# Kernel optimization log

Hardware: AMD Instinct MI355X
Metric: run time of the kernel (lower is better)

## Reference

```python
import jax, jax.numpy as jnp
import numpy as np

EPS = 1e-5

def _bn_eval(x, gamma, beta, mean, var):
    return (x - mean) * (gamma / jnp.sqrt(var + EPS)) + beta

def setup_inputs() -> dict:
    key = jax.random.key(0)
    ks = jax.random.split(key, 12)
    N, E, D, C, H = 100000, 1000000, 64, 32, 128
    fused = 4 * D + C  # 288
    z = jax.random.normal(ks[0], (N, D), dtype=jnp.float32)
    edge_index = jax.random.randint(ks[1], (2, E), 0, N, dtype=jnp.int64)
    edge_context = jax.random.normal(ks[2], (E, C), dtype=jnp.float32)
    W1 = jax.random.normal(ks[3], (fused, H), dtype=jnp.float32) / np.sqrt(fused)
    b1 = jnp.zeros((H,), jnp.float32)
    g1 = jnp.ones((H,), jnp.float32); be1 = jnp.zeros((H,), jnp.float32)
    m1 = jnp.zeros((H,), jnp.float32); v1 = jnp.ones((H,), jnp.float32)
    W2 = jax.random.normal(ks[4], (H, H // 2), dtype=jnp.float32) / np.sqrt(H)
    b2 = jnp.zeros((H // 2,), jnp.float32)
    g2 = jnp.ones((H // 2,), jnp.float32); be2 = jnp.zeros((H // 2,), jnp.float32)
    m2 = jnp.zeros((H // 2,), jnp.float32); v2 = jnp.ones((H // 2,), jnp.float32)
    W3 = jax.random.normal(ks[5], (H // 2, 1), dtype=jnp.float32) / np.sqrt(H // 2)
    b3 = jnp.zeros((1,), jnp.float32)
    return {"z": z, "edge_index": edge_index, "edge_context": edge_context,
            "W1": W1, "b1": b1, "g1": g1, "be1": be1, "m1": m1, "v1": v1,
            "W2": W2, "b2": b2, "g2": g2, "be2": be2, "m2": m2, "v2": v2,
            "W3": W3, "b3": b3}

def reference(z, edge_index, edge_context,
              W1, b1, g1, be1, m1, v1,
              W2, b2, g2, be2, m2, v2,
              W3, b3):
    # gather endpoint embeddings: [E, D]
    src = z[edge_index[0]]
    dst = z[edge_index[1]]
    # fused features: [E, 4*D + C]
    fused = jnp.concatenate([src, dst, src * dst, jnp.abs(src - dst), edge_context], axis=1)
    x = jax.nn.relu(_bn_eval(fused @ W1 + b1, g1, be1, m1, v1))
    x = jax.nn.relu(_bn_eval(x @ W2 + b2, g2, be2, m2, v2))
    return (x @ W3 + b3).reshape(-1)
```

## Files before the change

kernel.cpp:

```cpp
#include <hip/hip_runtime.h>
#include <hip/hip_bf16.h>

typedef __attribute__((ext_vector_type(8))) short bf16x8;
typedef __attribute__((ext_vector_type(4))) float f32x4;
typedef __attribute__((ext_vector_type(4))) unsigned int u32x4;
typedef __attribute__((ext_vector_type(2))) unsigned int u32x2;
typedef __attribute__((ext_vector_type(2))) __bf16 bf16x2v;

#define EPS 1e-5f

__device__ inline unsigned short f2bf(float x) {
  unsigned int u = __builtin_bit_cast(unsigned int, x);
  unsigned int r = (u + 0x7FFFu + ((u >> 16) & 1u)) >> 16;
  return (unsigned short)r;
}

__device__ inline unsigned int cvtpk(float a, float b) {
  bf16x2v v = {(__bf16)a, (__bf16)b};
  return __builtin_bit_cast(unsigned int, v);
}

__global__ void prep_kernel(const float* __restrict__ W1, const float* __restrict__ W2,
                            const float* __restrict__ b1, const float* __restrict__ g1,
                            const float* __restrict__ be1, const float* __restrict__ m1,
                            const float* __restrict__ v1,
                            const float* __restrict__ b2, const float* __restrict__ g2,
                            const float* __restrict__ be2, const float* __restrict__ m2,
                            const float* __restrict__ v2,
                            unsigned short* __restrict__ w1f, unsigned short* __restrict__ w2f,
                            float* __restrict__ sc) {
  int t = blockIdx.x * 256 + threadIdx.x;
  if (t < 36864) {
    int j = t & 7, l = (t >> 3) & 63, f = t >> 9;
    int kb = f >> 3, nb = f & 7;
    int rk = kb * 32 + ((l >> 4) << 3) + j;
    int cn = (nb << 4) + (l & 15);
    w1f[t] = f2bf(W1[rk * 128 + cn]);
  } else if (t < 45056) {
    int o = t - 36864;
    int j = o & 7, l = (o >> 3) & 63, f = o >> 9;
    int kb = f >> 2, nb = f & 3;
    int s = kb * 32 + ((l >> 4) << 3) + j;
    int rk = (s & 96) | ((s & 1) << 4) | ((s >> 1) & 15);
    int cn = (nb << 4) + (l & 15);
    w2f[o] = f2bf(W2[rk * 64 + cn]);
  } else if (t < 45184) {
    int j = t - 45056;
    float s = g1[j] * rsqrtf(v1[j] + EPS);
    sc[j] = s;
    sc[128 + j] = (b1[j] - m1[j]) * s + be1[j];
  } else if (t < 45248) {
    int j = t - 45184;
    float s = g2[j] * rsqrtf(v2[j] + EPS);
    sc[256 + j] = s;
    sc[320 + j] = (b2[j] - m2[j]) * s + be2[j];
  }
}

#define R_X1_OFF 81920
#define R_W2_OFF 114688
#define R_L3_OFF 131072
#define R_LDS_TOTAL 132096

#define WRITE_A_R()                                                                              \
  do {                                                                                           \
    const int rswz_ = (sr & 7) << 4;                                                             \
    char* rowp_ = AR + sr * 640;                                                                 \
    u32x4 s0_ = {cvtpk(sv0[0], sv0[1]), cvtpk(sv0[2], sv0[3]), cvtpk(sv1[0], sv1[1]),            \
                 cvtpk(sv1[2], sv1[3])};                                                         \
    u32x4 s1_ = {cvtpk(sv2[0], sv2[1]), cvtpk(sv2[2], sv2[3]), cvtpk(sv3[0], sv3[1]),            \
                 cvtpk(sv3[2], sv3[3])};                                                         \
    u32x4 d0_ = {cvtpk(dv0[0], dv0[1]), cvtpk(dv0[2], dv0[3]), cvtpk(dv1[0], dv1[1]),            \
                 cvtpk(dv1[2], dv1[3])};                                                         \
    u32x4 d1_ = {cvtpk(dv2[0], dv2[1]), cvtpk(dv2[2], dv2[3]), cvtpk(dv3[0], dv3[1]),            \
                 cvtpk(dv3[2], dv3[3])};                                                         \
    u32x4 p0_ = {cvtpk(sv0[0] * dv0[0], sv0[1] * dv0[1]), cvtpk(sv0[2] * dv0[2], sv0[3] * dv0[3]),\
                 cvtpk(sv1[0] * dv1[0], sv1[1] * dv1[1]), cvtpk(sv1[2] * dv1[2], sv1[3] * dv1[3])};\
    u32x4 p1_ = {cvtpk(sv2[0] * dv2[0], sv2[1] * dv2[1]), cvtpk(sv2[2] * dv2[2], sv2[3] * dv2[3]),\
                 cvtpk(sv3[0] * dv3[0], sv3[1] * dv3[1]), cvtpk(sv3[2] * dv3[2], sv3[3] * dv3[3])};\
    u32x4 a0_ = {cvtpk(fabsf(sv0[0] - dv0[0]), fabsf(sv0[1] - dv0[1])),                          \
                 cvtpk(fabsf(sv0[2] - dv0[2]), fabsf(sv0[3] - dv0[3])),                          \
                 cvtpk(fabsf(sv1[0] - dv1[0]), fabsf(sv1[1] - dv1[1])),                          \
                 cvtpk(fabsf(sv1[2] - dv1[2]), fabsf(sv1[3] - dv1[3]))};                         \
    u32x4 a1_ = {cvtpk(fabsf(sv2[0] - dv2[0]), fabsf(sv2[1] - dv2[1])),                          \
                 cvtpk(fabsf(sv2[2] - dv2[2]), fabsf(sv2[3] - dv2[3])),                          \
                 cvtpk(fabsf(sv3[0] - dv3[0]), fabsf(sv3[1] - dv3[1])),                          \
                 cvtpk(fabsf(sv3[2] - dv3[2]), fabsf(sv3[3] - dv3[3]))};                         \
    u32x4 c0_ = {cvtpk(cv0[0], cv0[1]), cvtpk(cv0[2], cv0[3]), cvtpk(cv1[0], cv1[1]),            \
                 cvtpk(cv1[2], cv1[3])};                                                         \
    *(u32x4*)(rowp_ + ((sh * 32) ^ rswz_)) = s0_;                                                \
    *(u32x4*)(rowp_ + ((sh * 32 + 16) ^ rswz_)) = s1_;                                           \
    *(u32x4*)(rowp_ + ((128 + sh * 32) ^ rswz_)) = d0_;                                          \
    *(u32x4*)(rowp_ + ((128 + sh * 32 + 16) ^ rswz_)) = d1_;                                     \
    *(u32x4*)(rowp_ + ((256 + sh * 32) ^ rswz_)) = p0_;                                          \
    *(u32x4*)(rowp_ + ((256 + sh * 32 + 16) ^ rswz_)) = p1_;                                     \
    *(u32x4*)(rowp_ + ((384 + sh * 32) ^ rswz_)) = a0_;                                          \
    *(u32x4*)(rowp_ + ((384 + sh * 32 + 16) ^ rswz_)) = a1_;                                     \
    *(u32x4*)(rowp_ + ((512 + sh * 16) ^ rswz_)) = c0_;                                          \
  } while (0)

#define GATHER_NEXT_R(tg)                                                                        \
  do {                                                                                           \
    const f32x4* zs_ = (const f32x4*)(z + ((size_t)i0n * 64 + sh * 16));                         \
    sv0 = zs_[0]; sv1 = zs_[1]; sv2 = zs_[2]; sv3 = zs_[3];                                      \
    const f32x4* zd_ = (const f32x4*)(z + ((size_t)i1n * 64 + sh * 16));                         \
    dv0 = zd_[0]; dv1 = zd_[1]; dv2 = zd_[2]; dv3 = zd_[3];                                      \
    int eg_ = ((tg) << 7) + sr;                                                                  \
    int esg_ = eg_ < E ? eg_ : E - 1;                                                            \
    const f32x4* cx_ = (const f32x4*)(ctx + (size_t)esg_ * 32 + sh * 8);                         \
    cv0 = cx_[0]; cv1 = cx_[1];                                                                  \
    int tn_ = (tg) + grid;                                                                       \
    if (tn_ >= nblk) tn_ = (tg);                                                                 \
    int en_ = (tn_ << 7) + sr;                                                                   \
    int esn_ = en_ < E ? en_ : E - 1;                                                            \
    i0n = ei[esn_];                                                                              \
    i1n = ei[E + esn_];                                                                          \
  } while (0)

#define MFMA16(A, B, C) __builtin_amdgcn_mfma_f32_16x16x32_bf16((A), (B), (C), 0, 0, 0)

#define L1STEP_R(KB, BB0, BB1)                                                                   \
  do {                                                                                           \
    bf16x8 a0_ = *(const bf16x8*)(ap0 + (((KB) * 64 + g * 16) ^ aswz));                          \
    bf16x8 a1_ = *(const bf16x8*)(ap1 + (((KB) * 64 + g * 16) ^ aswz));                          \
    bf16x8 a2_ = *(const bf16x8*)(ap2 + (((KB) * 64 + g * 16) ^ aswz));                          \
    bf16x8 a3_ = *(const bf16x8*)(ap3 + (((KB) * 64 + g * 16) ^ aswz));                          \
    acc00 = MFMA16(a0_, BB0, acc00); acc01 = MFMA16(a0_, BB1, acc01);                            \
    acc10 = MFMA16(a1_, BB0, acc10); acc11 = MFMA16(a1_, BB1, acc11);                            \
    acc20 = MFMA16(a2_, BB0, acc20); acc21 = MFMA16(a2_, BB1, acc21);                            \
    acc30 = MFMA16(a3_, BB0, acc30); acc31 = MFMA16(a3_, BB1, acc31);                            \
  } while (0)

#define X1W_R(MF, ACA, ACB)                                                                      \
  do {                                                                                           \
    _Pragma("unroll")                                                                            \
    for (int j = 0; j < 4; j++) {                                                                \
      int row_ = wr * 64 + (MF) * 16 + 4 * g + j;                                                \
      unsigned int p_ = cvtpk(fmaxf(ACA[j] * s1v0 + c1v0, 0.f),                                  \
                              fmaxf(ACB[j] * s1v1 + c1v1, 0.f));                                 \
      *(unsigned int*)(X1 + row_ * 256 + (xoff ^ ((row_ & 7) << 4))) = p_;                       \
    }                                                                                            \
  } while (0)

#define L2STEP_R(KB)                                                                             \
  do {                                                                                           \
    bf16x8 xa_ = *(const bf16x8*)(xp0 + (((KB) * 64 + g * 16) ^ aswz));                          \
    bf16x8 xb_ = *(const bf16x8*)(xp1 + (((KB) * 64 + g * 16) ^ aswz));                          \
    bf16x8 bg_ = *(const bf16x8*)(W2L + (((KB) * 4 + w2c * 2 + 0) * 64 + lane) * 16);            \
    bf16x8 bh_ = *(const bf16x8*)(W2L + (((KB) * 4 + w2c * 2 + 1) * 64 + lane) * 16);            \
    acc2A0 = MFMA16(xa_, bg_, acc2A0); acc2A1 = MFMA16(xa_, bh_, acc2A1);                        \
    acc2B0 = MFMA16(xb_, bg_, acc2B0); acc2B1 = MFMA16(xb_, bh_, acc2B1);                        \
  } while (0)

__global__ __launch_bounds__(512, 1) void fused_kernel_r(
    const float* __restrict__ z, const int* __restrict__ ei, const float* __restrict__ ctx,
    const unsigned short* __restrict__ w1f, const unsigned short* __restrict__ w2f,
    const float* __restrict__ sc, const float* __restrict__ w3, const float* __restrict__ b3,
    float* __restrict__ out, int E, int nblk) {
  extern __shared__ char lds[];
  char* AR = lds;
  char* X1 = lds + R_X1_OFF;
  char* W2L = lds + R_W2_OFF;
  float* l3 = (float*)(lds + R_L3_OFF);

  const int tid = threadIdx.x;
  const int lane = tid & 63, wave = tid >> 6;
  const int g = lane >> 4, lq = lane & 15;
  const int wr = wave >> 2, wc = wave & 3;
  const int w2r = wave >> 1, w2c = wave & 1;
  const int sr = tid >> 2, sh = tid & 3;
  const int grid = gridDim.x;
  const int aswz = (lq & 7) << 4;

  ((f32x4*)W2L)[tid] = ((const f32x4*)w2f)[tid];
  ((f32x4*)W2L)[512 + tid] = ((const f32x4*)w2f)[512 + tid];

  const int col0 = wc * 32 + lq;
  const float s1v0 = sc[col0], c1v0 = sc[128 + col0];
  const float s1v1 = sc[col0 + 16], c1v1 = sc[128 + col0 + 16];
  const int colA = w2c * 32 + lq;
  const float s2A = sc[256 + colA], c2A = sc[320 + colA];
  const float s2B = sc[256 + colA + 16], c2B = sc[320 + colA + 16];
  const float w3A = w3[colA], w3B = w3[colA + 16];
  const float b3v = b3[0];
  const int xoff = wc * 64 + lq * 4;

  const bf16x8* W1G = (const bf16x8*)w1f;
  bf16x8 w1r0 = W1G[(0 * 8 + wc * 2 + 0) * 64 + lane], w1s0 = W1G[(0 * 8 + wc * 2 + 1) * 64 + lane];
  bf16x8 w1r1 = W1G[(1 * 8 + wc * 2 + 0) * 64 + lane], w1s1 = W1G[(1 * 8 + wc * 2 + 1) * 64 + lane];
  bf16x8 w1r2 = W1G[(2 * 8 + wc * 2 + 0) * 64 + lane], w1s2 = W1G[(2 * 8 + wc * 2 + 1) * 64 + lane];
  bf16x8 w1r3 = W1G[(3 * 8 + wc * 2 + 0) * 64 + lane], w1s3 = W1G[(3 * 8 + wc * 2 + 1) * 64 + lane];
  bf16x8 w1r4 = W1G[(4 * 8 + wc * 2 + 0) * 64 + lane], w1s4 = W1G[(4 * 8 + wc * 2 + 1) * 64 + lane];
  bf16x8 w1r5 = W1G[(5 * 8 + wc * 2 + 0) * 64 + lane], w1s5 = W1G[(5 * 8 + wc * 2 + 1) * 64 + lane];
  bf16x8 w1r6 = W1G[(6 * 8 + wc * 2 + 0) * 64 + lane], w1s6 = W1G[(6 * 8 + wc * 2 + 1) * 64 + lane];
  bf16x8 w1r7 = W1G[(7 * 8 + wc * 2 + 0) * 64 + lane], w1s7 = W1G[(7 * 8 + wc * 2 + 1) * 64 + lane];
  bf16x8 w1r8 = W1G[(8 * 8 + wc * 2 + 0) * 64 + lane], w1s8 = W1G[(8 * 8 + wc * 2 + 1) * 64 + lane];

  f32x4 sv0, sv1, sv2, sv3, dv0, dv1, dv2, dv3, cv0, cv1;
  int i0n, i1n;
  int t = blockIdx.x;

  {
    int e = (t << 7) + sr;
    int es = e < E ? e : E - 1;
    int a0 = ei[es], a1 = ei[E + es];
    const f32x4* cx = (const f32x4*)(ctx + (size_t)es * 32 + sh * 8);
    cv0 = cx[0]; cv1 = cx[1];
    const f32x4* zs = (const f32x4*)(z + ((size_t)a0 * 64 + sh * 16));
    sv0 = zs[0]; sv1 = zs[1]; sv2 = zs[2]; sv3 = zs[3];
    const f32x4* zd = (const f32x4*)(z + ((size_t)a1 * 64 + sh * 16));
    dv0 = zd[0]; dv1 = zd[1]; dv2 = zd[2]; dv3 = zd[3];
    int tn = t + grid;
    if (tn >= nblk) tn = t;
    int en = (tn << 7) + sr;
    int esn = en < E ? en : E - 1;
    i0n = ei[esn];
    i1n = ei[E + esn];
  }
  WRITE_A_R();
  {
    int tn = t + grid;
    if (tn >= nblk) tn = t;
    GATHER_NEXT_R(tn);
  }
  __syncthreads();

  for (; t < nblk; t += grid) {
    f32x4 acc00 = {0.f, 0.f, 0.f, 0.f}, acc01 = acc00, acc10 = acc00, acc11 = acc00;
    f32x4 acc20 = acc00, acc21 = acc00, acc30 = acc00, acc31 = acc00;
    const char* ap0 = AR + (wr * 64 + 0 * 16 + lq) * 640;
    const char* ap1 = AR + (wr * 64 + 1 * 16 + lq) * 640;
    const char* ap2 = AR + (wr * 64 + 2 * 16 + lq) * 640;
    const char* ap3 = AR + (wr * 64 + 3 * 16 + lq) * 640;
    L1STEP_R(0, w1r0, w1s0);
    L1STEP_R(1, w1r1, w1s1);
    L1STEP_R(2, w1r2, w1s2);
    L1STEP_R(3, w1r3, w1s3);
    L1STEP_R(4, w1r4, w1s4);
    L1STEP_R(5, w1r5, w1s5);
    L1STEP_R(6, w1r6, w1s6);
    L1STEP_R(7, w1r7, w1s7);
    L1STEP_R(8, w1r8, w1s8);
    __syncthreads();

    WRITE_A_R();
    {
      int tn2 = t + 2 * grid;
      if (tn2 >= nblk) tn2 = t + grid < nblk ? t + grid : t;
      GATHER_NEXT_R(tn2);
    }
    X1W_R(0, acc00, acc01);
    X1W_R(1, acc10, acc11);
    X1W_R(2, acc20, acc21);
    X1W_R(3, acc30, acc31);
    __syncthreads();

    f32x4 acc2A0 = {0.f, 0.f, 0.f, 0.f}, acc2A1 = acc2A0, acc2B0 = acc2A0, acc2B1 = acc2A0;
    const char* xp0 = X1 + (w2r * 32 + lq) * 256;
    const char* xp1 = xp0 + 4096;
    L2STEP_R(0);
    L2STEP_R(1);
    L2STEP_R(2);
    L2STEP_R(3);

    {
#pragma unroll
      for (int j = 0; j < 4; j++) {
        float pA = fmaxf(acc2A0[j] * s2A + c2A, 0.f) * w3A +
                   fmaxf(acc2A1[j] * s2B + c2B, 0.f) * w3B;
        pA += __shfl_xor(pA, 1);
        pA += __shfl_xor(pA, 2);
        pA += __shfl_xor(pA, 4);
        pA += __shfl_xor(pA, 8);
        float pB = fmaxf(acc2B0[j] * s2A + c2A, 0.f) * w3A +
                   fmaxf(acc2B1[j] * s2B + c2B, 0.f) * w3B;
        pB += __shfl_xor(pB, 1);
        pB += __shfl_xor(pB, 2);
        pB += __shfl_xor(pB, 4);
        pB += __shfl_xor(pB, 8);
        if (lq == 0) {
          l3[(w2r * 32 + 4 * g + j) * 2 + w2c] = pA;
          l3[(w2r * 32 + 16 + 4 * g + j) * 2 + w2c] = pB;
        }
      }
    }
    __syncthreads();

    if (tid < 128) {
      int e = (t << 7) + tid;
      if (e < E) out[e] = l3[tid * 2] + l3[tid * 2 + 1] + b3v;
    }
  }
}

#define F_SC_OFF 73728
#define F_A_OFF 75776
#define F_L3_OFF 157696
#define F_LDS_TOTAL 158720

#define WRITE_A_F()                                                                              \
  do {                                                                                           \
    const int rswz_ = (sr & 7) << 4;                                                             \
    char* rowp_ = AR + sr * 640;                                                                 \
    u32x4 ps_ = {cvtpk(sv0[0], sv0[1]), cvtpk(sv0[2], sv0[3]), cvtpk(sv1[0], sv1[1]),            \
                 cvtpk(sv1[2], sv1[3])};                                                         \
    u32x4 pd_ = {cvtpk(dv0[0], dv0[1]), cvtpk(dv0[2], dv0[3]), cvtpk(dv1[0], dv1[1]),            \
                 cvtpk(dv1[2], dv1[3])};                                                         \
    u32x4 pp_ = {cvtpk(sv0[0] * dv0[0], sv0[1] * dv0[1]), cvtpk(sv0[2] * dv0[2], sv0[3] * dv0[3]),\
                 cvtpk(sv1[0] * dv1[0], sv1[1] * dv1[1]), cvtpk(sv1[2] * dv1[2], sv1[3] * dv1[3])};\
    u32x4 pa_ = {cvtpk(fabsf(sv0[0] - dv0[0]), fabsf(sv0[1] - dv0[1])),                          \
                 cvtpk(fabsf(sv0[2] - dv0[2]), fabsf(sv0[3] - dv0[3])),                          \
                 cvtpk(fabsf(sv1[0] - dv1[0]), fabsf(sv1[1] - dv1[1])),                          \
                 cvtpk(fabsf(sv1[2] - dv1[2]), fabsf(sv1[3] - dv1[3]))};                         \
    u32x2 pc_ = {cvtpk(cv[0], cv[1]), cvtpk(cv[2], cv[3])};                                      \
    *(u32x4*)(rowp_ + ((sh * 16) ^ rswz_)) = ps_;                                                \
    *(u32x4*)(rowp_ + ((128 + sh * 16) ^ rswz_)) = pd_;                                          \
    *(u32x4*)(rowp_ + ((256 + sh * 16) ^ rswz_)) = pp_;                                          \
    *(u32x4*)(rowp_ + ((384 + sh * 16) ^ rswz_)) = pa_;                                          \
    *(u32x2*)(rowp_ + 512 + ((sh * 8) ^ rswz_)) = pc_;                                           \
  } while (0)

#define GATHER_NEXT_F(tg)                                                                        \
  do {                                                                                           \
    const f32x4* zs_ = (const f32x4*)(z + ((size_t)i0n * 64 + sh * 8));                          \
    sv0 = zs_[0];                                                                                \
    sv1 = zs_[1];                                                                                \
    const f32x4* zd_ = (const f32x4*)(z + ((size_t)i1n * 64 + sh * 8));                          \
    dv0 = zd_[0];                                                                                \
    dv1 = zd_[1];                                                                                \
    int eg_ = ((tg) << 7) + sr;                                                                  \
    int esg_ = eg_ < E ? eg_ : E - 1;                                                            \
    cv = *(const f32x4*)(ctx + (size_t)esg_ * 32 + sh * 4);                                      \
    int tn_ = (tg) + grid;                                                                       \
    if (tn_ >= nblk) tn_ = (tg);                                                                 \
    int en_ = (tn_ << 7) + sr;                                                                   \
    int esn_ = en_ < E ? en_ : E - 1;                                                            \
    i0n = ei[esn_];                                                                              \
    i1n = ei[E + esn_];                                                                          \
  } while (0)

__global__ __launch_bounds__(1024, 4) void fused_kernel_f(
    const float* __restrict__ z, const int* __restrict__ ei, const float* __restrict__ ctx,
    const unsigned short* __restrict__ w1f, const unsigned short* __restrict__ w2f,
    const float* __restrict__ sc, const float* __restrict__ w3, const float* __restrict__ b3,
    float* __restrict__ out, int E, int nblk) {
  extern __shared__ char lds[];
  char* W1L = lds;
  float* SC = (float*)(lds + F_SC_OFF);
  char* AR = lds + F_A_OFF;
  char* X1 = lds + F_A_OFF;
  float* l3 = (float*)(lds + F_L3_OFF);

  const int tid = threadIdx.x;
  const int lane = tid & 63, wave = tid >> 6;
  const int g = lane >> 4, lq = lane & 15;
  const int wr = wave >> 2, wc = wave & 3;
  const int w2r = wave >> 1, w2c = wave & 1;
  const int sr = tid >> 3, sh = tid & 7;
  const int grid = gridDim.x;

  {
    const f32x4* s = (const f32x4*)w1f;
    f32x4* d = (f32x4*)W1L;
#pragma unroll
    for (int i = 0; i < 4; i++) d[i * 1024 + tid] = s[i * 1024 + tid];
    if (tid < 512) d[4096 + tid] = s[4096 + tid];
    if (tid < 128) {
      SC[tid] = sc[tid];
      SC[128 + tid] = sc[128 + tid];
    } else if (tid < 192) {
      int j = tid - 128;
      SC[256 + j] = sc[256 + j];
      SC[320 + j] = sc[320 + j];
      SC[384 + j] = w3[j];
    } else if (tid == 192) {
      SC[448] = b3[0];
    }
  }

  bf16x8 w2g0, w2g1, w2g2, w2g3, w2h0, w2h1, w2h2, w2h3;
  {
    const bf16x8* W2G = (const bf16x8*)w2f;
    w2g0 = W2G[(0 * 4 + w2c * 2 + 0) * 64 + lane];
    w2h0 = W2G[(0 * 4 + w2c * 2 + 1) * 64 + lane];
    w2g1 = W2G[(1 * 4 + w2c * 2 + 0) * 64 + lane];
    w2h1 = W2G[(1 * 4 + w2c * 2 + 1) * 64 + lane];
    w2g2 = W2G[(2 * 4 + w2c * 2 + 0) * 64 + lane];
    w2h2 = W2G[(2 * 4 + w2c * 2 + 1) * 64 + lane];
    w2g3 = W2G[(3 * 4 + w2c * 2 + 0) * 64 + lane];
    w2h3 = W2G[(3 * 4 + w2c * 2 + 1) * 64 + lane];
  }

  f32x4 sv0, sv1, dv0, dv1, cv;
  int i0n, i1n;
  int t = blockIdx.x;

  {
    int e = (t << 7) + sr;
    int es = e < E ? e : E - 1;
    int a0 = ei[es], a1 = ei[E + es];
    cv = *(const f32x4*)(ctx + (size_t)es * 32 + sh * 4);
    const f32x4* zs = (const f32x4*)(z + ((size_t)a0 * 64 + sh * 8));
    sv0 = zs[0];
    sv1 = zs[1];
    const f32x4* zd = (const f32x4*)(z + ((size_t)a1 * 64 + sh * 8));
    dv0 = zd[0];
    dv1 = zd[1];
    int tn = t + grid;
    if (tn >= nblk) tn = t;
    int en = (tn << 7) + sr;
    int esn = en < E ? en : E - 1;
    i0n = ei[esn];
    i1n = ei[E + esn];
  }
  WRITE_A_F();
  {
    int tn = t + grid;
    if (tn >= nblk) tn = t;
    GATHER_NEXT_F(tn);
  }
  __syncthreads();

  for (; t < nblk; t += grid) {
    f32x4 acc00 = {0.f, 0.f, 0.f, 0.f}, acc01 = acc00, acc10 = acc00, acc11 = acc00;
    const bf16x8* W1F = (const bf16x8*)W1L;
    const int row0 = wr * 32 + lq, row1 = row0 + 16;
    const int swz0 = (row0 & 7) << 4, swz1 = (row1 & 7) << 4;
    const char* ap0 = AR + row0 * 640;
    const char* ap1 = AR + row1 * 640;
#pragma unroll
    for (int kb = 0; kb < 9; kb++) {
      bf16x8 a0 = *(const bf16x8*)(ap0 + ((kb * 64 + g * 16) ^ swz0));
      bf16x8 a1 = *(const bf16x8*)(ap1 + ((kb * 64 + g * 16) ^ swz1));
      bf16x8 b0 = W1F[(kb * 8 + wc * 2 + 0) * 64 + lane];
      bf16x8 b1 = W1F[(kb * 8 + wc * 2 + 1) * 64 + lane];
      acc00 = MFMA16(a0, b0, acc00);
      acc01 = MFMA16(a0, b1, acc01);
      acc10 = MFMA16(a1, b0, acc10);
      acc11 = MFMA16(a1, b1, acc11);
    }
    __syncthreads();

    {
      const int col0 = wc * 32 + lq;
      const float s1v0 = SC[col0], c1v0 = SC[128 + col0];
      const float s1v1 = SC[col0 + 16], c1v1 = SC[128 + col0 + 16];
      const int xoff = wc * 64 + lq * 4;
#pragma unroll
      for (int j = 0; j < 4; j++) {
        int rowa = wr * 32 + 4 * g + j;
        unsigned int pA = cvtpk(fmaxf(acc00[j] * s1v0 + c1v0, 0.f),
                                fmaxf(acc01[j] * s1v1 + c1v1, 0.f));
        *(unsigned int*)(X1 + rowa * 256 + (xoff ^ ((rowa & 7) << 4))) = pA;
        int rowb = rowa + 16;
        unsigned int pB = cvtpk(fmaxf(acc10[j] * s1v0 + c1v0, 0.f),
                                fmaxf(acc11[j] * s1v1 + c1v1, 0.f));
        *(unsigned int*)(X1 + rowb * 256 + (xoff ^ ((rowb & 7) << 4))) = pB;
      }
    }
    __syncthreads();

    f32x4 acc2A = {0.f, 0.f, 0.f, 0.f}, acc2B = acc2A;
    {
      const int row = w2r * 16 + lq;
      const int swz = (row & 7) << 4;
      const char* xp = X1 + row * 256;
      bf16x8 a0 = *(const bf16x8*)(xp + ((0 * 64 + g * 16) ^ swz));
      acc2A = MFMA16(a0, w2g0, acc2A);
      acc2B = MFMA16(a0, w2h0, acc2B);
      bf16x8 a1 = *(const bf16x8*)(xp + ((1 * 64 + g * 16) ^ swz));
      acc2A = MFMA16(a1, w2g1, acc2A);
      acc2B = MFMA16(a1, w2h1, acc2B);
      bf16x8 a2 = *(const bf16x8*)(xp + ((2 * 64 + g * 16) ^ swz));
      acc2A = MFMA16(a2, w2g2, acc2A);
      acc2B = MFMA16(a2, w2h2, acc2B);
      bf16x8 a3 = *(const bf16x8*)(xp + ((3 * 64 + g * 16) ^ swz));
      acc2A = MFMA16(a3, w2g3, acc2A);
      acc2B = MFMA16(a3, w2h3, acc2B);
    }

    const int colA = w2c * 32 + lq, colB = colA + 16;
    const float s2A = SC[256 + colA], c2A = SC[320 + colA];
    const float s2B = SC[256 + colB], c2B = SC[320 + colB];
    const float w3A = SC[384 + colA], w3B = SC[384 + colB];
#pragma unroll
    for (int j = 0; j < 4; j++) {
      float vA = fmaxf(acc2A[j] * s2A + c2A, 0.f);
      float vB = fmaxf(acc2B[j] * s2B + c2B, 0.f);
      float p = vA * w3A + vB * w3B;
      p += __shfl_xor(p, 1);
      p += __shfl_xor(p, 2);
      p += __shfl_xor(p, 4);
      p += __shfl_xor(p, 8);
      if (lq == 0) l3[(w2r * 16 + 4 * g + j) * 2 + w2c] = p;
    }
    __syncthreads();

    WRITE_A_F();
    {
      int tn2 = t + 2 * grid;
      if (tn2 >= nblk) tn2 = t + grid < nblk ? t + grid : t;
      GATHER_NEXT_F(tn2);
    }
    if (tid < 128) {
      int e = (t << 7) + tid;
      if (e < E) out[e] = l3[tid * 2] + l3[tid * 2 + 1] + SC[448];
    }
    __syncthreads();
  }
}

extern "C" void kernel_launch(void* const* d_in, const int* in_sizes, int n_in,
                              void* d_out, int out_size, void* d_ws, size_t ws_size,
                              hipStream_t stream) {
  const float* z = (const float*)d_in[0];
  const int* ei = (const int*)d_in[1];
  const float* ctx = (const float*)d_in[2];
  const float* W1 = (const float*)d_in[3];
  const float* b1 = (const float*)d_in[4];
  const float* g1 = (const float*)d_in[5];
  const float* be1 = (const float*)d_in[6];
  const float* m1 = (const float*)d_in[7];
  const float* v1 = (const float*)d_in[8];
  const float* W2 = (const float*)d_in[9];
  const float* b2 = (const float*)d_in[10];
  const float* g2 = (const float*)d_in[11];
  const float* be2 = (const float*)d_in[12];
  const float* m2 = (const float*)d_in[13];
  const float* v2 = (const float*)d_in[14];
  const float* W3 = (const float*)d_in[15];
  const float* b3 = (const float*)d_in[16];
  float* out = (float*)d_out;
  const int E = out_size;

  unsigned short* w1f = (unsigned short*)d_ws;
  unsigned short* w2f = (unsigned short*)((char*)d_ws + 73728);
  float* sc = (float*)((char*)d_ws + 90112);

  prep_kernel<<<177, 256, 0, stream>>>(W1, W2, b1, g1, be1, m1, v1,
                                       b2, g2, be2, m2, v2, w1f, w2f, sc);

  const int nblk = (E + 127) >> 7;

  hipFuncAttributes attr;
  bool use_r = false;
  if (hipFuncGetAttributes(&attr, (const void*)fused_kernel_r) == hipSuccess) {
    use_r = (attr.localSizeBytes < 16);
  }

  if (use_r) {
    (void)hipFuncSetAttribute((const void*)fused_kernel_r,
                              hipFuncAttributeMaxDynamicSharedMemorySize, R_LDS_TOTAL);
    fused_kernel_r<<<256, 512, R_LDS_TOTAL, stream>>>(z, ei, ctx, w1f, w2f, sc, W3, b3,
                                                      out, E, nblk);
  } else {
    (void)hipFuncSetAttribute((const void*)fused_kernel_f,
                              hipFuncAttributeMaxDynamicSharedMemorySize, F_LDS_TOTAL);
    fused_kernel_f<<<256, 1024, F_LDS_TOTAL, stream>>>(z, ei, ctx, w1f, w2f, sc, W3, b3,
                                                       out, E, nblk);
  }
}
```

Measured before the change: 137.2 us.

## Stage W1 in LDS instead of registers and alias A/X1/W2 buffers

```diff
diff --git a/kernel.cpp b/kernel.cpp
--- a/kernel.cpp
+++ b/kernel.cpp
@@ -19,6 +19,8 @@
   bf16x2v v = {(__bf16)a, (__bf16)b};
   return __builtin_bit_cast(unsigned int, v);
 }
+
+#define MFMA16(A, B, C) __builtin_amdgcn_mfma_f32_16x16x32_bf16((A), (B), (C), 0, 0, 0)
 
 __global__ void prep_kernel(const float* __restrict__ W1, const float* __restrict__ W2,
                             const float* __restrict__ b1, const float* __restrict__ g1,
@@ -57,12 +59,11 @@
   }
 }
 
-#define R_X1_OFF 81920
-#define R_W2_OFF 114688
-#define R_L3_OFF 131072
-#define R_LDS_TOTAL 132096
-
-#define WRITE_A_R()                                                                              \
+#define P_A_OFF 73728
+#define P_L3_OFF 155648
+#define P_LDS_TOTAL 156672
+
+#define WRITE_A_P()                                                                              \
   do {                                                                                           \
     const int rswz_ = (sr & 7) << 4;                                                             \
     char* rowp_ = AR + sr * 640;                                                                 \
@@ -99,7 +100,7 @@
     *(u32x4*)(rowp_ + ((512 + sh * 16) ^ rswz_)) = c0_;                                          \
   } while (0)
 
-#define GATHER_NEXT_R(tg)                                                                        \
+#define GATHER_NEXT_P(tg)                                                                        \
   do {                                                                                           \
     const f32x4* zs_ = (const f32x4*)(z + ((size_t)i0n * 64 + sh * 16));                         \
     sv0 = zs_[0]; sv1 = zs_[1]; sv2 = zs_[2]; sv3 = zs_[3];                                      \
@@ -117,21 +118,21 @@
     i1n = ei[E + esn_];                                                                          \
   } while (0)
 
-#define MFMA16(A, B, C) __builtin_amdgcn_mfma_f32_16x16x32_bf16((A), (B), (C), 0, 0, 0)
-
-#define L1STEP_R(KB, BB0, BB1)                                                                   \
-  do {                                                                                           \
+#define L1STEP_P(KB)                                                                             \
+  do {                                                                                           \
+    bf16x8 b0_ = W1F[((KB) * 8 + wc * 2 + 0) * 64 + lane];                                       \
+    bf16x8 b1_ = W1F[((KB) * 8 + wc * 2 + 1) * 64 + lane];                                       \
     bf16x8 a0_ = *(const bf16x8*)(ap0 + (((KB) * 64 + g * 16) ^ aswz));                          \
     bf16x8 a1_ = *(const bf16x8*)(ap1 + (((KB) * 64 + g * 16) ^ aswz));                          \
     bf16x8 a2_ = *(const bf16x8*)(ap2 + (((KB) * 64 + g * 16) ^ aswz));                          \
     bf16x8 a3_ = *(const bf16x8*)(ap3 + (((KB) * 64 + g * 16) ^ aswz));                          \
-    acc00 = MFMA16(a0_, BB0, acc00); acc01 = MFMA16(a0_, BB1, acc01);                            \
-    acc10 = MFMA16(a1_, BB0, acc10); acc11 = MFMA16(a1_, BB1, acc11);                            \
-    acc20 = MFMA16(a2_, BB0, acc20); acc21 = MFMA16(a2_, BB1, acc21);                            \
-    acc30 = MFMA16(a3_, BB0, acc30); acc31 = MFMA16(a3_, BB1, acc31);                            \
-  } while (0)
-
-#define X1W_R(MF, ACA, ACB)                                                                      \
+    acc00 = MFMA16(a0_, b0_, acc00); acc01 = MFMA16(a0_, b1_, acc01);                            \
+    acc10 = MFMA16(a1_, b0_, acc10); acc11 = MFMA16(a1_, b1_, acc11);                            \
+    acc20 = MFMA16(a2_, b0_, acc20); acc21 = MFMA16(a2_, b1_, acc21);                            \
+    acc30 = MFMA16(a3_, b0_, acc30); acc31 = MFMA16(a3_, b1_, acc31);                            \
+  } while (0)
+
+#define X1W_P(MF, ACA, ACB)                                                                      \
   do {                                                                                           \
     _Pragma("unroll")                                                                            \
     for (int j = 0; j < 4; j++) {                                                                \
@@ -142,26 +143,27 @@
     }                                                                                            \
   } while (0)
 
-#define L2STEP_R(KB)                                                                             \
+#define L2STEP_P(KB)                                                                             \
   do {                                                                                           \
     bf16x8 xa_ = *(const bf16x8*)(xp0 + (((KB) * 64 + g * 16) ^ aswz));                          \
     bf16x8 xb_ = *(const bf16x8*)(xp1 + (((KB) * 64 + g * 16) ^ aswz));                          \
-    bf16x8 bg_ = *(const bf16x8*)(W2L + (((KB) * 4 + w2c * 2 + 0) * 64 + lane) * 16);            \
-    bf16x8 bh_ = *(const bf16x8*)(W2L + (((KB) * 4 + w2c * 2 + 1) * 64 + lane) * 16);            \
+    bf16x8 bg_ = W2F[((KB) * 4 + w2c * 2 + 0) * 64 + lane];                                      \
+    bf16x8 bh_ = W2F[((KB) * 4 + w2c * 2 + 1) * 64 + lane];                                      \
     acc2A0 = MFMA16(xa_, bg_, acc2A0); acc2A1 = MFMA16(xa_, bh_, acc2A1);                        \
     acc2B0 = MFMA16(xb_, bg_, acc2B0); acc2B1 = MFMA16(xb_, bh_, acc2B1);                        \
   } while (0)
 
-__global__ __launch_bounds__(512, 1) void fused_kernel_r(
+__global__ __launch_bounds__(512) void fused_kernel_p(
     const float* __restrict__ z, const int* __restrict__ ei, const float* __restrict__ ctx,
     const unsigned short* __restrict__ w1f, const unsigned short* __restrict__ w2f,
     const float* __restrict__ sc, const float* __restrict__ w3, const float* __restrict__ b3,
     float* __restrict__ out, int E, int nblk) {
   extern __shared__ char lds[];
-  char* AR = lds;
-  char* X1 = lds + R_X1_OFF;
-  char* W2L = lds + R_W2_OFF;
-  float* l3 = (float*)(lds + R_L3_OFF);
+  char* W1L = lds;
+  char* AR = lds + P_A_OFF;
+  char* X1 = lds + P_A_OFF;
+  char* W2L = lds + P_A_OFF + 32768;
+  float* l3 = (float*)(lds + P_L3_OFF);
 
   const int tid = threadIdx.x;
   const int lane = tid & 63, wave = tid >> 6;
@@ -172,29 +174,21 @@
   const int grid = gridDim.x;
   const int aswz = (lq & 7) << 4;
 
-  ((f32x4*)W2L)[tid] = ((const f32x4*)w2f)[tid];
-  ((f32x4*)W2L)[512 + tid] = ((const f32x4*)w2f)[512 + tid];
-
-  const int col0 = wc * 32 + lq;
-  const float s1v0 = sc[col0], c1v0 = sc[128 + col0];
-  const float s1v1 = sc[col0 + 16], c1v1 = sc[128 + col0 + 16];
+  {
+    const f32x4* s1p = (const f32x4*)w1f;
+    f32x4* d1p = (f32x4*)W1L;
+#pragma unroll
+    for (int i = 0; i < 9; i++) d1p[i * 512 + tid] = s1p[i * 512 + tid];
+  }
+
+  const float s1v0 = sc[wc * 32 + lq], c1v0 = sc[128 + wc * 32 + lq];
+  const float s1v1 = sc[wc * 32 + 16 + lq], c1v1 = sc[128 + wc * 32 + 16 + lq];
   const int colA = w2c * 32 + lq;
   const float s2A = sc[256 + colA], c2A = sc[320 + colA];
   const float s2B = sc[256 + colA + 16], c2B = sc[320 + colA + 16];
   const float w3A = w3[colA], w3B = w3[colA + 16];
   const float b3v = b3[0];
   const int xoff = wc * 64 + lq * 4;
-
-  const bf16x8* W1G = (const bf16x8*)w1f;
-  bf16x8 w1r0 = W1G[(0 * 8 + wc * 2 + 0) * 64 + lane], w1s0 = W1G[(0 * 8 + wc * 2 + 1) * 64 + lane];
-  bf16x8 w1r1 = W1G[(1 * 8 + wc * 2 + 0) * 64 + lane], w1s1 = W1G[(1 * 8 + wc * 2 + 1) * 64 + lane];
-  bf16x8 w1r2 = W1G[(2 * 8 + wc * 2 + 0) * 64 + lane], w1s2 = W1G[(2 * 8 + wc * 2 + 1) * 64 + lane];
-  bf16x8 w1r3 = W1G[(3 * 8 + wc * 2 + 0) * 64 + lane], w1s3 = W1G[(3 * 8 + wc * 2 + 1) * 64 + lane];
-  bf16x8 w1r4 = W1G[(4 * 8 + wc * 2 + 0) * 64 + lane], w1s4 = W1G[(4 * 8 + wc * 2 + 1) * 64 + lane];
-  bf16x8 w1r5 = W1G[(5 * 8 + wc * 2 + 0) * 64 + lane], w1s5 = W1G[(5 * 8 + wc * 2 + 1) * 64 + lane];
-  bf16x8 w1r6 = W1G[(6 * 8 + wc * 2 + 0) * 64 + lane], w1s6 = W1G[(6 * 8 + wc * 2 + 1) * 64 + lane];
-  bf16x8 w1r7 = W1G[(7 * 8 + wc * 2 + 0) * 64 + lane], w1s7 = W1G[(7 * 8 + wc * 2 + 1) * 64 + lane];
-  bf16x8 w1r8 = W1G[(8 * 8 + wc * 2 + 0) * 64 + lane], w1s8 = W1G[(8 * 8 + wc * 2 + 1) * 64 + lane];
 
   f32x4 sv0, sv1, sv2, sv3, dv0, dv1, dv2, dv3, cv0, cv1;
   int i0n, i1n;
@@ -217,14 +211,16 @@
     i0n = ei[esn];
     i1n = ei[E + esn];
   }
-  WRITE_A_R();
+  WRITE_A_P();
   {
     int tn = t + grid;
     if (tn >= nblk) tn = t;
-    GATHER_NEXT_R(tn);
+    GATHER_NEXT_P(tn);
   }
   __syncthreads();
 
+  const bf16x8* W1F = (const bf16x8*)W1L;
+  const bf16x8* W2F = (const bf16x8*)W2L;
   for (; t < nblk; t += grid) {
     f32x4 acc00 = {0.f, 0.f, 0.f, 0.f}, acc01 = acc00, acc10 = acc00, acc11 = acc00;
     f32x4 acc20 = acc00, acc21 = acc00, acc30 = acc00, acc31 = acc00;
@@ -232,64 +228,64 @@
     const char* ap1 = AR + (wr * 64 + 1 * 16 + lq) * 640;
     const char* ap2 = AR + (wr * 64 + 2 * 16 + lq) * 640;
     const char* ap3 = AR + (wr * 64 + 3 * 16 + lq) * 640;
-    L1STEP_R(0, w1r0, w1s0);
-    L1STEP_R(1, w1r1, w1s1);
-    L1STEP_R(2, w1r2, w1s2);
-    L1STEP_R(3, w1r3, w1s3);
-    L1STEP_R(4, w1r4, w1s4);
-    L1STEP_R(5, w1r5, w1s5);
-    L1STEP_R(6, w1r6, w1s6);
-    L1STEP_R(7, w1r7, w1s7);
-    L1STEP_R(8, w1r8, w1s8);
-    __syncthreads();
-
-    WRITE_A_R();
+    L1STEP_P(0);
+    L1STEP_P(1);
+    L1STEP_P(2);
+    L1STEP_P(3);
+    L1STEP_P(4);
+    L1STEP_P(5);
+    L1STEP_P(6);
+    L1STEP_P(7);
+    L1STEP_P(8);
+    __syncthreads();
+
+    ((f32x4*)W2L)[tid] = ((const f32x4*)w2f)[tid];
+    ((f32x4*)W2L)[512 + tid] = ((const f32x4*)w2f)[512 + tid];
+    X1W_P(0, acc00, acc01);
+    X1W_P(1, acc10, acc11);
+    X1W_P(2, acc20, acc21);
+    X1W_P(3, acc30, acc31);
+    __syncthreads();
+
+    f32x4 acc2A0 = {0.f, 0.f, 0.f, 0.f}, acc2A1 = acc2A0, acc2B0 = acc2A0, acc2B1 = acc2A0;
+    const char* xp0 = X1 + (w2r * 32 + lq) * 256;
+    const char* xp1 = xp0 + 4096;
+    L2STEP_P(0);
+    L2STEP_P(1);
+    L2STEP_P(2);
+    L2STEP_P(3);
+#pragma unroll
+    for (int j = 0; j < 4; j++) {
+      float pA = fmaxf(acc2A0[j] * s2A + c2A, 0.f) * w3A +
+                 fmaxf(acc2A1[j] * s2B + c2B, 0.f) * w3B;
+      pA += __shfl_xor(pA, 1);
+      pA += __shfl_xor(pA, 2);
+      pA += __shfl_xor(pA, 4);
+      pA += __shfl_xor(pA, 8);
+      float pB = fmaxf(acc2B0[j] * s2A + c2A, 0.f) * w3A +
+                 fmaxf(acc2B1[j] * s2B + c2B, 0.f) * w3B;
+      pB += __shfl_xor(pB, 1);
+      pB += __shfl_xor(pB, 2);
+      pB += __shfl_xor(pB, 4);
+      pB += __shfl_xor(pB, 8);
+      if (lq == 0) {
+        l3[(w2r * 32 + 4 * g + j) * 2 + w2c] = pA;
+        l3[(w2r * 32 + 16 + 4 * g + j) * 2 + w2c] = pB;
+      }
+    }
+    __syncthreads();
+
+    WRITE_A_P();
     {
       int tn2 = t + 2 * grid;
       if (tn2 >= nblk) tn2 = t + grid < nblk ? t + grid : t;
-      GATHER_NEXT_R(tn2);
-    }
-    X1W_R(0, acc00, acc01);
-    X1W_R(1, acc10, acc11);
-    X1W_R(2, acc20, acc21);
-    X1W_R(3, acc30, acc31);
-    __syncthreads();
-
-    f32x4 acc2A0 = {0.f, 0.f, 0.f, 0.f}, acc2A1 = acc2A0, acc2B0 = acc2A0, acc2B1 = acc2A0;
-    const char* xp0 = X1 + (w2r * 32 + lq) * 256;
-    const char* xp1 = xp0 + 4096;
-    L2STEP_R(0);
-    L2STEP_R(1);
-    L2STEP_R(2);
-    L2STEP_R(3);
-
-    {
-#pragma unroll
-      for (int j = 0; j < 4; j++) {
-        float pA = fmaxf(acc2A0[j] * s2A + c2A, 0.f) * w3A +
-                   fmaxf(acc2A1[j] * s2B + c2B, 0.f) * w3B;
-        pA += __shfl_xor(pA, 1);
-        pA += __shfl_xor(pA, 2);
-        pA += __shfl_xor(pA, 4);
-        pA += __shfl_xor(pA, 8);
-        float pB = fmaxf(acc2B0[j] * s2A + c2A, 0.f) * w3A +
-                   fmaxf(acc2B1[j] * s2B + c2B, 0.f) * w3B;
-        pB += __shfl_xor(pB, 1);
-        pB += __shfl_xor(pB, 2);
-        pB += __shfl_xor(pB, 4);
-        pB += __shfl_xor(pB, 8);
-        if (lq == 0) {
-          l3[(w2r * 32 + 4 * g + j) * 2 + w2c] = pA;
-          l3[(w2r * 32 + 16 + 4 * g + j) * 2 + w2c] = pB;
-        }
-      }
-    }
-    __syncthreads();
-
+      GATHER_NEXT_P(tn2);
+    }
     if (tid < 128) {
       int e = (t << 7) + tid;
       if (e < E) out[e] = l3[tid * 2] + l3[tid * 2 + 1] + b3v;
     }
+    __syncthreads();
   }
 }
 
@@ -543,15 +539,15 @@
   const int nblk = (E + 127) >> 7;
 
   hipFuncAttributes attr;
-  bool use_r = false;
-  if (hipFuncGetAttributes(&attr, (const void*)fused_kernel_r) == hipSuccess) {
-    use_r = (attr.localSizeBytes < 16);
-  }
-
-  if (use_r) {
-    (void)hipFuncSetAttribute((const void*)fused_kernel_r,
-                              hipFuncAttributeMaxDynamicSharedMemorySize, R_LDS_TOTAL);
-    fused_kernel_r<<<256, 512, R_LDS_TOTAL, stream>>>(z, ei, ctx, w1f, w2f, sc, W3, b3,
+  bool use_p = false;
+  if (hipFuncGetAttributes(&attr, (const void*)fused_kernel_p) == hipSuccess) {
+    use_p = (attr.localSizeBytes < 16);
+  }
+
+  if (use_p) {
+    (void)hipFuncSetAttribute((const void*)fused_kernel_p,
+                              hipFuncAttributeMaxDynamicSharedMemorySize, P_LDS_TOTAL);
+    fused_kernel_p<<<256, 512, P_LDS_TOTAL, stream>>>(z, ei, ctx, w1f, w2f, sc, W3, b3,
                                                       out, E, nblk);
   } else {
     (void)hipFuncSetAttribute((const void*)fused_kernel_f,
```

Result: slower. 149.7 us (+9.1%).
